# Kernel optimization log

Measured on AMD Instinct MI355X. Metric: run time of the kernel, lower is better.

Reference implementation:

```python
import jax, jax.numpy as jnp
import numpy as np

DEPTH, HEADS, DIM_HEAD, DIM, MLP, PATCH_DIM, NP_, NC = 8, 8, 64, 512, 2048, 512, 1024, 2
INNER = HEADS * DIM_HEAD
SCALE = DIM_HEAD ** -0.5
EPS = 1e-5

def layernorm(x, s, b):
    m = x.mean(-1, keepdims=True)
    v = ((x - m) ** 2).mean(-1, keepdims=True)
    return (x - m) * jax.lax.rsqrt(v + EPS) * s + b

def setup_inputs() -> dict:
    key = jax.random.key(0)
    ks = jax.random.split(key, 24)
    g = lambda k, sh, sc=0.02: jax.random.normal(k, sh, dtype=jnp.float32) * sc
    return {
        "img": jax.random.normal(ks[0], (4, NP_, PATCH_DIM), dtype=jnp.float32),
        "embed_w": g(ks[1], (PATCH_DIM, DIM)), "embed_b": jnp.zeros((DIM,), jnp.float32),
        "pos_emb": g(ks[2], (1, NP_ + 1, DIM), 1.0), "cls_token": g(ks[3], (1, 1, DIM), 1.0),
        "ln1_s": jnp.ones((DEPTH, DIM), jnp.float32), "ln1_b": jnp.zeros((DEPTH, DIM), jnp.float32),
        "qkv_w": g(ks[4], (DEPTH, DIM, 3 * INNER)),
        "out_w": g(ks[5], (DEPTH, INNER, DIM)), "out_b": jnp.zeros((DEPTH, DIM), jnp.float32),
        "ln2_s": jnp.ones((DEPTH, DIM), jnp.float32), "ln2_b": jnp.zeros((DEPTH, DIM), jnp.float32),
        "ff_w1": g(ks[6], (DEPTH, DIM, MLP)), "ff_b1": jnp.zeros((DEPTH, MLP), jnp.float32),
        "ff_w2": g(ks[7], (DEPTH, MLP, DIM)), "ff_b2": jnp.zeros((DEPTH, DIM), jnp.float32),
        "head_ln_s": jnp.ones((DIM,), jnp.float32), "head_ln_b": jnp.zeros((DIM,), jnp.float32),
        "head_w": g(ks[8], (DIM, NC)), "head_b": jnp.zeros((NC,), jnp.float32),
    }

def reference(img, embed_w, embed_b, pos_emb, cls_token, ln1_s, ln1_b, qkv_w, out_w, out_b,
              ln2_s, ln2_b, ff_w1, ff_b1, ff_w2, ff_b2, head_ln_s, head_ln_b, head_w, head_b):
    B, N, _ = img.shape
    x = img @ embed_w + embed_b                       # [B, N, DIM]
    cls = jnp.broadcast_to(cls_token, (B, 1, DIM))
    x = jnp.concatenate([cls, x], axis=1) + pos_emb[:, :N + 1]
    for l in range(DEPTH):
        h = layernorm(x, ln1_s[l], ln1_b[l])
        qkv = h @ qkv_w[l]                            # [B, N+1, 3*INNER]
        q, k, v = jnp.split(qkv, 3, axis=-1)
        rh = lambda t: t.reshape(B, N + 1, HEADS, DIM_HEAD).transpose(0, 2, 1, 3)
        q, k, v = rh(q), rh(k), rh(v)                 # [B, H, N+1, Dh]
        dots = jnp.einsum('bhnd,bhmd->bhnm', q, k) * SCALE
        attn = jax.nn.softmax(dots, axis=-1)
        o = jnp.einsum('bhnm,bhmd->bhnd', attn, v)
        o = o.transpose(0, 2, 1, 3).reshape(B, N + 1, INNER)
        x = o @ out_w[l] + out_b[l] + x
        h = layernorm(x, ln2_s[l], ln2_b[l])
        h = jax.nn.gelu(h @ ff_w1[l] + ff_b1[l], approximate=False)
        x = h @ ff_w2[l] + ff_b2[l] + x
    x = x[:, 0]                                       # cls pooling
    x = layernorm(x, head_ln_s, head_ln_b)
    return (jax.nn.sigmoid(x @ head_w + head_b),)
```

## Files before the change

kernel.cpp:

```cpp
#include <hip/hip_runtime.h>
#include <math.h>
#include <stdint.h>

#define NHEADS   8
#define DHEAD    64
#define DIMM     512
#define MLPD     2048
#define NPATCH   1024
#define NTOK     1025
#define BATCH    4
#define ROWS     (BATCH*NTOK)
#define TOKPAD   1088
#define NCHUNK   17
#define CSPLIT   9
#define QSC      0.180336881f
#define LN_EPS   1e-5f

typedef __attribute__((ext_vector_type(8))) short short8;
typedef __attribute__((ext_vector_type(4))) float f32x4;

__device__ __forceinline__ unsigned short f2bf(float f) {
  union { float f; unsigned u; } c; c.f = f;
  unsigned u = c.u;
  return (unsigned short)((u + 0x7fffu + ((u >> 16) & 1u)) >> 16);
}
__device__ __forceinline__ unsigned short f2bf_fast(float f) {
  union { float f; unsigned u; } c; c.f = f;
  return (unsigned short)((c.u + 0x8000u) >> 16);
}
__device__ __forceinline__ float bf2f(unsigned short b) {
  union { unsigned u; float f; } c; c.u = (unsigned)b << 16;
  return c.f;
}

__device__ __forceinline__ float wsum(float v) {
#pragma unroll
  for (int o = 32; o > 0; o >>= 1) v += __shfl_xor(v, o, 64);
  return v;
}

__device__ __forceinline__ void gl_lds16(const void* g, const void* l) {
  __builtin_amdgcn_global_load_lds(
      (const __attribute__((address_space(1))) unsigned int*)(uintptr_t)g,
      (__attribute__((address_space(3))) unsigned int*)(unsigned int)(uintptr_t)l,
      16, 0, 0);
}

template <int TM, int TN, int WR, int WC, bool ACOMB>
__global__ __launch_bounds__(256) void mgemm_k(
    const unsigned short* __restrict__ A, const unsigned short* __restrict__ Bt,
    const float* __restrict__ bias, const float* __restrict__ res,
    void* __restrict__ Cout, int M, int N, int K, int flags,
    unsigned short* __restrict__ vTout, const float* __restrict__ mlc,
    const float* __restrict__ posp)
{
  constexpr int AF = TM / WR / 16;
  constexpr int BF = TN / WC / 16;
  constexpr int AG = TM / 32;
  constexpr int BG = TN / 32;
  __shared__ unsigned short sA[2][TM * 64];
  __shared__ unsigned short sB[2][TN * 64];
  const int tid = threadIdx.x;
  const int w = tid >> 6, lane = tid & 63;
  const int quad = lane >> 4, l15 = lane & 15;
  const int m0 = blockIdx.y * TM, n0 = blockIdx.x * TN;
  const int wrow = (w / WC) * (TM / WR);
  const int wcol = (w % WC) * (TN / WC);
  const int lrow = lane >> 3;
  const int lkg = (lane & 7) ^ lrow;

  size_t abase[AG], bbase[BG];
  int arow[AG];
#pragma unroll
  for (int g = 0; g < AG; g++) {
    int grp = w * AG + g;
    int ar = m0 + grp * 8 + lrow; ar = ar < M ? ar : M - 1;
    arow[g] = ar;
    abase[g] = (size_t)ar * K + lkg * 8;
  }
#pragma unroll
  for (int g = 0; g < BG; g++) {
    int grp = w * BG + g;
    int br = n0 + grp * 8 + lrow;
    bbase[g] = (size_t)br * K + lkg * 8;
  }

  auto stageB = [&](int k0, int buf) {
#pragma unroll
    for (int g = 0; g < BG; g++)
      gl_lds16(Bt + bbase[g] + k0, &sB[buf][(w * BG + g) * 512]);
  };
  auto stageA_dma = [&](int k0, int buf) {
#pragma unroll
    for (int g = 0; g < AG; g++)
      gl_lds16(A + abase[g] + k0, &sA[buf][(w * AG + g) * 512]);
  };

  uint4 ra0[AG], ra1[AG];
  float rl0[AG], rl1[AG];
  auto loadAC = [&](int k0) {
    const int h = k0 >> 6;
#pragma unroll
    for (int g = 0; g < AG; g++) {
      size_t off = abase[g] + k0;
      ra0[g] = *(const uint4*)(A + off);
      ra1[g] = *(const uint4*)(A + (size_t)ROWS * DIMM + off);
      int b = arow[g] / NTOK, tok = arow[g] - b * NTOK;
      int bh = b * 8 + h;
      rl0[g] = mlc[(size_t)bh * NTOK + tok];
      rl1[g] = mlc[(size_t)(32 + bh) * NTOK + tok];
    }
  };
  auto writeAC = [&](int buf) {
#pragma unroll
    for (int g = 0; g < AG; g++) {
      float inv = 1.0f / (rl0[g] + rl1[g]);
      const unsigned short* p0 = (const unsigned short*)&ra0[g];
      const unsigned short* p1 = (const unsigned short*)&ra1[g];
      alignas(16) unsigned short o[8];
#pragma unroll
      for (int i = 0; i < 8; i++)
        o[i] = f2bf((bf2f(p0[i]) + bf2f(p1[i])) * inv);
      *(uint4*)&sA[buf][(w * AG + g) * 512 + lane * 8] = *(const uint4*)o;
    }
  };

  f32x4 acc[AF][BF];
#pragma unroll
  for (int i = 0; i < AF; i++)
#pragma unroll
    for (int j = 0; j < BF; j++) { f32x4 z = {0.f, 0.f, 0.f, 0.f}; acc[i][j] = z; }

  if (ACOMB) { stageB(0, 0); loadAC(0); writeAC(0); }
  else       { stageA_dma(0, 0); stageB(0, 0); }

  const int nsteps = K >> 6;
  for (int step = 0; step < nsteps; step++) {
    const int buf = step & 1;
    __syncthreads();
    if (step + 1 < nsteps) {
      stageB((step + 1) << 6, buf ^ 1);
      if (ACOMB) loadAC((step + 1) << 6);
      else       stageA_dma((step + 1) << 6, buf ^ 1);
    }
#pragma unroll
    for (int kk = 0; kk < 2; kk++) {
      short8 af[AF], bfr[BF];
#pragma unroll
      for (int i = 0; i < AF; i++) {
        int r = wrow + i * 16 + l15;
        af[i] = *(const short8*)&sA[buf][r * 64 + (((kk * 4 + quad) ^ (lane & 7)) << 3)];
      }
#pragma unroll
      for (int j = 0; j < BF; j++) {
        int r = wcol + j * 16 + l15;
        bfr[j] = *(const short8*)&sB[buf][r * 64 + (((kk * 4 + quad) ^ (lane & 7)) << 3)];
      }
#pragma unroll
      for (int i = 0; i < AF; i++)
#pragma unroll
        for (int j = 0; j < BF; j++)
          acc[i][j] = __builtin_amdgcn_mfma_f32_16x16x32_bf16(af[i], bfr[j], acc[i][j], 0, 0, 0);
    }
    if (ACOMB && step + 1 < nsteps) writeAC(buf ^ 1);
  }

  const bool do_gelu = flags & 1;
  const bool out_bf  = flags & 2;
  const bool embedf  = flags & 4;
#pragma unroll
  for (int i = 0; i < AF; i++) {
#pragma unroll
    for (int j = 0; j < BF; j++) {
      const int col = n0 + wcol + j * 16 + l15;
      const bool vcol = (vTout != nullptr) && (col >= 1024);
      alignas(8) unsigned short vb[4];
#pragma unroll
      for (int rg = 0; rg < 4; rg++) {
        int row = m0 + wrow + i * 16 + quad * 4 + rg;
        if (row >= M) continue;
        float v = acc[i][j][rg];
        if (bias) v += bias[col];
        if (do_gelu) v = 0.5f * v * (1.0f + erff(v * 0.70710678118654752f));
        if (res) v += res[(size_t)row * N + col];
        if (embedf) {
          int bb = row >> 10, t = (row & 1023) + 1;
          ((float*)Cout)[((size_t)(bb * NTOK + t)) * N + col] =
              v + posp[(size_t)t * N + col];
        } else if (out_bf) {
          unsigned short bv = f2bf(v);
          vb[rg] = bv;
          if (!vcol) ((unsigned short*)Cout)[(size_t)row * N + col] = bv;
        } else {
          ((float*)Cout)[(size_t)row * N + col] = v;
        }
      }
      if (vcol) {
        const int hcol = col - 1024, h = hcol >> 6, d = hcol & 63;
#pragma unroll
        for (int rg = 0; rg < 4; rg++) {
          int row = m0 + wrow + i * 16 + quad * 4 + rg;
          if (row >= M) continue;
          int bb = row / NTOK, tok = row - bb * NTOK;
          vTout[((size_t)(bb * 8 + h) * 64 + d) * TOKPAD + tok] = vb[rg];
        }
      }
    }
  }
}

__global__ __launch_bounds__(256) void attn_k(
    const unsigned short* __restrict__ qkv, const unsigned short* __restrict__ vT,
    unsigned short* __restrict__ po, float* __restrict__ ml)
{
  __shared__ unsigned short ps[64 * 64];
  __shared__ unsigned short ks[2][64 * 64];
  __shared__ unsigned short vs[2][64 * 64];
  const int bh = blockIdx.x, b = bh >> 3, h = bh & 7;
  const int q0 = blockIdx.y * 64;
  const int split = blockIdx.z;
  const int tid = threadIdx.x, w = tid >> 6, lane = tid & 63;
  const int quad = lane >> 4, l15 = lane & 15;
  const int lrow = lane >> 3, lkg = (lane & 7) ^ lrow;
  const unsigned short* qbase = qkv + (size_t)(b * NTOK) * 1536 + h * 64;
  const unsigned short* kbase = qbase + 512;
  const unsigned short* vtb   = vT + (size_t)bh * 64 * TOKPAD;

  auto stage_kv = [&](int c0, int buf) {
#pragma unroll
    for (int g = 0; g < 2; g++) {
      int grp = w * 2 + g;
      int tok = c0 + grp * 8 + lrow; tok = tok < NTOK ? tok : NTOK - 1;
      gl_lds16(kbase + (size_t)tok * 1536 + lkg * 8, &ks[buf][grp * 512]);
      int d = grp * 8 + lrow;
      gl_lds16(vtb + (size_t)d * TOKPAD + c0 + lkg * 8, &vs[buf][grp * 512]);
    }
  };

  const int cbeg = split ? CSPLIT : 0;
  const int cend = split ? NCHUNK : CSPLIT;
  stage_kv(cbeg * 64, 0);

  int qr = q0 + w * 16 + l15; qr = qr < NTOK ? qr : NTOK - 1;
  const unsigned short* qrow = qbase + (size_t)qr * 1536;
  short8 aq[2];
  aq[0] = *(const short8*)(qrow + quad * 8);
  aq[1] = *(const short8*)(qrow + 32 + quad * 8);
#pragma unroll
  for (int k = 0; k < 2; k++)
#pragma unroll
    for (int i = 0; i < 8; i++)
      aq[k][i] = (short)f2bf(bf2f((unsigned short)aq[k][i]) * QSC);

  short8 ones;
#pragma unroll
  for (int i = 0; i < 8; i++) ones[i] = (short)0x3F80;

  f32x4 Oa[4];
#pragma unroll
  for (int n = 0; n < 4; n++) { f32x4 z = {0.f, 0.f, 0.f, 0.f}; Oa[n] = z; }
  float lst[4] = {0.f, 0.f, 0.f, 0.f};

  for (int c = cbeg; c < cend; c++) {
    const int c0 = c * 64;
    const int buf = (c - cbeg) & 1;
    __syncthreads();
    if (c + 1 < cend) stage_kv(c0 + 64, buf ^ 1);

    f32x4 sa[4];
#pragma unroll
    for (int n = 0; n < 4; n++) {
      f32x4 s = {0.f, 0.f, 0.f, 0.f};
#pragma unroll
      for (int kk = 0; kk < 2; kk++) {
        short8 bk = *(const short8*)&ks[buf][(n * 16 + l15) * 64 + (((kk * 4 + quad) ^ (lane & 7)) << 3)];
        s = __builtin_amdgcn_mfma_f32_16x16x32_bf16(aq[kk], bk, s, 0, 0, 0);
      }
      sa[n] = s;
    }

    if (c0 + 64 > NTOK) {
#pragma unroll
      for (int n = 0; n < 4; n++) {
        bool oob = (c0 + n * 16 + l15) >= NTOK;
#pragma unroll
        for (int rg = 0; rg < 4; rg++)
          if (oob) sa[n][rg] = -1e30f;
      }
    }

#pragma unroll
    for (int n = 0; n < 4; n++)
#pragma unroll
      for (int rg = 0; rg < 4; rg++) {
        int row = w * 16 + quad * 4 + rg;
        int key = n * 16 + l15;
        ps[row * 64 + ((((key >> 3) ^ (row & 7)) & 7) << 3) + (key & 7)] =
            f2bf_fast(exp2f(sa[n][rg]));
      }

    short8 ap[2];
#pragma unroll
    for (int kk = 0; kk < 2; kk++)
      ap[kk] = *(const short8*)&ps[(w * 16 + l15) * 64 + (((kk * 4 + quad) ^ (lane & 7)) << 3)];

    f32x4 lsum = {0.f, 0.f, 0.f, 0.f};
#pragma unroll
    for (int kk = 0; kk < 2; kk++)
      lsum = __builtin_amdgcn_mfma_f32_16x16x32_bf16(ap[kk], ones, lsum, 0, 0, 0);
#pragma unroll
    for (int rg = 0; rg < 4; rg++) lst[rg] += lsum[rg];

#pragma unroll
    for (int n = 0; n < 4; n++) {
      f32x4 o = Oa[n];
#pragma unroll
      for (int kk = 0; kk < 2; kk++) {
        short8 bv = *(const short8*)&vs[buf][(n * 16 + l15) * 64 + (((kk * 4 + quad) ^ (lane & 7)) << 3)];
        o = __builtin_amdgcn_mfma_f32_16x16x32_bf16(ap[kk], bv, o, 0, 0, 0);
      }
      Oa[n] = o;
    }
  }

  unsigned short* pob = po + (size_t)split * ROWS * DIMM;
#pragma unroll
  for (int n = 0; n < 4; n++)
#pragma unroll
    for (int rg = 0; rg < 4; rg++) {
      int tok = q0 + w * 16 + quad * 4 + rg;
      if (tok < NTOK)
        pob[(size_t)(b * NTOK + tok) * DIMM + h * 64 + n * 16 + l15] = f2bf(Oa[n][rg]);
    }
  if (l15 == 0) {
#pragma unroll
    for (int rg = 0; rg < 4; rg++) {
      int tok = q0 + w * 16 + quad * 4 + rg;
      if (tok < NTOK)
        ml[(size_t)(split * 32 + bh) * NTOK + tok] = lst[rg];
    }
  }
}

__global__ __launch_bounds__(256) void ln_k(
    const float* __restrict__ X, const float* __restrict__ s,
    const float* __restrict__ b, unsigned short* __restrict__ Y, int nrows)
{
  const int w = threadIdx.x >> 6, lane = threadIdx.x & 63;
  const int row = blockIdx.x * 4 + w;
  if (row >= nrows) return;
  const float* x = X + (size_t)row * DIMM;
  float4 v0 = *(const float4*)(x + lane * 8);
  float4 v1 = *(const float4*)(x + lane * 8 + 4);
  float xv[8] = {v0.x, v0.y, v0.z, v0.w, v1.x, v1.y, v1.z, v1.w};
  float sum = 0.f, sq = 0.f;
#pragma unroll
  for (int i = 0; i < 8; i++) { sum += xv[i]; sq += xv[i] * xv[i]; }
  sum = wsum(sum); sq = wsum(sq);
  const float mean = sum * (1.0f / DIMM);
  const float var  = sq * (1.0f / DIMM) - mean * mean;
  const float r    = rsqrtf(var + LN_EPS);
  alignas(16) unsigned short tmp[8];
#pragma unroll
  for (int i = 0; i < 8; i++) {
    int d = lane * 8 + i;
    tmp[i] = f2bf((xv[i] - mean) * r * s[d] + b[d]);
  }
  *(uint4*)&Y[(size_t)row * DIMM + lane * 8] = *(const uint4*)tmp;
}

#define CLS_B   8
#define IMG_B   2048
#define TC0     (CLS_B + IMG_B)
#define TQKV    (TC0 + 256)
#define TOUT    (TQKV + 6144)
#define TFF1    (TOUT + 2048)
#define TFF2    (TFF1 + 8192)
#define TEND    (TFF2 + 8192)

__global__ __launch_bounds__(256) void prep_k(
    const float* __restrict__ embed_w, const float* __restrict__ qkv_w,
    const float* __restrict__ out_w, const float* __restrict__ ff1_w,
    const float* __restrict__ ff2_w,
    unsigned short* __restrict__ wt_embed, unsigned short* __restrict__ wt_qkv,
    unsigned short* __restrict__ wt_out, unsigned short* __restrict__ wt_ff1,
    unsigned short* __restrict__ wt_ff2,
    const float* __restrict__ img, unsigned short* __restrict__ img_bf,
    const float* __restrict__ cls, const float* __restrict__ pos,
    float* __restrict__ x)
{
  __shared__ float tl[32][33];
  const int bid = blockIdx.x, tid = threadIdx.x;
  if (bid < CLS_B) {
    int idx = bid * 256 + tid;
    int b = idx >> 9, d = idx & 511;
    x[(size_t)b * NTOK * DIMM + d] = cls[d] + pos[d];
    return;
  }
  if (bid < TC0) {
    int i = (bid - CLS_B) * 256 + tid;
    float4 v = ((const float4*)img)[i];
    alignas(8) unsigned short o[4] = {f2bf(v.x), f2bf(v.y), f2bf(v.z), f2bf(v.w)};
    ((uint2*)img_bf)[i] = *(const uint2*)o;
    return;
  }
  const float* W; unsigned short* Wt; int K, N, t;
  if (bid < TQKV)      { W = embed_w; Wt = wt_embed; K = 512;  N = 512;  t = bid - TC0;  }
  else if (bid < TOUT) { W = qkv_w;   Wt = wt_qkv;   K = 512;  N = 1536; t = bid - TQKV; }
  else if (bid < TFF1) { W = out_w;   Wt = wt_out;   K = 512;  N = 512;  t = bid - TOUT; }
  else if (bid < TFF2) { W = ff1_w;   Wt = wt_ff1;   K = 512;  N = 2048; t = bid - TFF1; }
  else                 { W = ff2_w;   Wt = wt_ff2;   K = 2048; N = 512;  t = bid - TFF2; }
  const int ntx = N >> 5;
  const int tpz = ntx * (K >> 5);
  const int z = t / tpz, r = t - z * tpz;
  const int n0 = (r % ntx) << 5, k0 = (r / ntx) << 5;
  const size_t off = (size_t)z * K * N;
  const float* Wz = W + off;
  unsigned short* Wtz = Wt + off;
  const int tx = tid & 31, ty = tid >> 5;
#pragma unroll
  for (int i = 0; i < 4; i++)
    tl[ty + 8 * i][tx] = Wz[(size_t)(k0 + ty + 8 * i) * N + n0 + tx];
  __syncthreads();
#pragma unroll
  for (int i = 0; i < 4; i++) {
    int n = ty + 8 * i;
    Wtz[(size_t)(n0 + n) * K + k0 + tx] = f2bf(tl[tx][n]);
  }
}

__global__ __launch_bounds__(256) void head_k(
    const float* __restrict__ X, const float* __restrict__ s,
    const float* __restrict__ bln, const float* __restrict__ W,
    const float* __restrict__ bh, float* __restrict__ out)
{
  const int w = threadIdx.x >> 6, lane = threadIdx.x & 63;
  if (w >= BATCH) return;
  const float* x = X + (size_t)w * NTOK * DIMM;
  float4 v0 = *(const float4*)(x + lane * 8);
  float4 v1 = *(const float4*)(x + lane * 8 + 4);
  float xv[8] = {v0.x, v0.y, v0.z, v0.w, v1.x, v1.y, v1.z, v1.w};
  float sum = 0.f, sq = 0.f;
#pragma unroll
  for (int i = 0; i < 8; i++) { sum += xv[i]; sq += xv[i] * xv[i]; }
  sum = wsum(sum); sq = wsum(sq);
  const float mean = sum * (1.0f / DIMM);
  const float var  = sq * (1.0f / DIMM) - mean * mean;
  const float r    = rsqrtf(var + LN_EPS);
  float l0 = 0.f, l1 = 0.f;
#pragma unroll
  for (int i = 0; i < 8; i++) {
    int d = lane * 8 + i;
    float xn = (xv[i] - mean) * r * s[d] + bln[d];
    l0 = fmaf(xn, W[d * 2 + 0], l0);
    l1 = fmaf(xn, W[d * 2 + 1], l1);
  }
  l0 = wsum(l0); l1 = wsum(l1);
  if (lane == 0) {
    out[w * 2 + 0] = 1.0f / (1.0f + expf(-(l0 + bh[0])));
    out[w * 2 + 1] = 1.0f / (1.0f + expf(-(l1 + bh[1])));
  }
}

extern "C" void kernel_launch(void* const* d_in, const int* in_sizes, int n_in,
                              void* d_out, int out_size, void* d_ws, size_t ws_size,
                              hipStream_t stream)
{
  const float* img       = (const float*)d_in[0];
  const float* embed_w   = (const float*)d_in[1];
  const float* embed_b   = (const float*)d_in[2];
  const float* pos_emb   = (const float*)d_in[3];
  const float* cls_token = (const float*)d_in[4];
  const float* ln1_s     = (const float*)d_in[5];
  const float* ln1_b     = (const float*)d_in[6];
  const float* qkv_w     = (const float*)d_in[7];
  const float* out_w     = (const float*)d_in[8];
  const float* out_b     = (const float*)d_in[9];
  const float* ln2_s     = (const float*)d_in[10];
  const float* ln2_b     = (const float*)d_in[11];
  const float* ff_w1     = (const float*)d_in[12];
  const float* ff_b1     = (const float*)d_in[13];
  const float* ff_w2     = (const float*)d_in[14];
  const float* ff_b2     = (const float*)d_in[15];
  const float* head_ln_s = (const float*)d_in[16];
  const float* head_ln_b = (const float*)d_in[17];
  const float* head_w    = (const float*)d_in[18];
  const float* head_b    = (const float*)d_in[19];
  float* out = (float*)d_out;

  char* p = (char*)d_ws;
  auto alloc = [&](size_t bytes) { char* r = p; p += (bytes + 255) & ~(size_t)255; return r; };

  unsigned short* wt_embed = (unsigned short*)alloc((size_t)512 * 512 * 2);
  unsigned short* wt_qkv   = (unsigned short*)alloc((size_t)8 * 1536 * 512 * 2);
  unsigned short* wt_out   = (unsigned short*)alloc((size_t)8 * 512 * 512 * 2);
  unsigned short* wt_ff1   = (unsigned short*)alloc((size_t)8 * 2048 * 512 * 2);
  unsigned short* wt_ff2   = (unsigned short*)alloc((size_t)8 * 512 * 2048 * 2);
  unsigned short* img_bf   = (unsigned short*)alloc((size_t)4096 * 512 * 2);
  float*          x        = (float*)alloc((size_t)ROWS * DIMM * 4);
  unsigned short* h        = (unsigned short*)alloc((size_t)ROWS * DIMM * 2);
  unsigned short* vTb      = (unsigned short*)alloc((size_t)32 * 64 * TOKPAD * 2);
  unsigned short* po       = (unsigned short*)alloc((size_t)2 * ROWS * DIMM * 2);
  float*          mlb      = (float*)alloc((size_t)2 * 32 * NTOK * 4);
  char*           big      = alloc((size_t)ROWS * MLPD * 2);
  unsigned short* qkvb     = (unsigned short*)big;
  unsigned short* ffh      = (unsigned short*)big;

  dim3 blk(256);

  prep_k<<<TEND, blk, 0, stream>>>(
      embed_w, qkv_w, out_w, ff_w1, ff_w2,
      wt_embed, wt_qkv, wt_out, wt_ff1, wt_ff2,
      img, img_bf, cls_token, pos_emb, x);

  mgemm_k<32, 64, 2, 2, false><<<dim3(8, 128), blk, 0, stream>>>(
      img_bf, wt_embed, embed_b, nullptr, x, 4096, 512, 512, 4,
      nullptr, nullptr, pos_emb);

  const int mt32 = (ROWS + 31) / 32;
  for (int l = 0; l < 8; l++) {
    ln_k<<<(ROWS + 3) / 4, blk, 0, stream>>>(
        x, ln1_s + l * DIMM, ln1_b + l * DIMM, h, ROWS);
    mgemm_k<32, 64, 2, 2, false><<<dim3(24, mt32), blk, 0, stream>>>(
        h, wt_qkv + (size_t)l * 1536 * 512, nullptr, nullptr,
        qkvb, ROWS, 1536, 512, 2, vTb, nullptr, nullptr);
    attn_k<<<dim3(32, 17, 2), blk, 0, stream>>>(qkvb, vTb, po, mlb);
    mgemm_k<32, 64, 2, 2, true><<<dim3(8, mt32), blk, 0, stream>>>(
        po, wt_out + (size_t)l * 512 * 512, out_b + l * DIMM, x,
        x, ROWS, 512, 512, 0, nullptr, mlb, nullptr);
    ln_k<<<(ROWS + 3) / 4, blk, 0, stream>>>(
        x, ln2_s + l * DIMM, ln2_b + l * DIMM, h, ROWS);
    mgemm_k<32, 64, 2, 2, false><<<dim3(32, mt32), blk, 0, stream>>>(
        h, wt_ff1 + (size_t)l * 2048 * 512, ff_b1 + l * MLPD, nullptr,
        ffh, ROWS, 2048, 512, 1 | 2, nullptr, nullptr, nullptr);
    mgemm_k<32, 64, 2, 2, false><<<dim3(8, mt32), blk, 0, stream>>>(
        ffh, wt_ff2 + (size_t)l * 512 * 2048, ff_b2 + l * DIMM, x,
        x, ROWS, 512, 2048, 0, nullptr, nullptr, nullptr);
  }

  head_k<<<1, blk, 0, stream>>>(x, head_ln_s, head_ln_b, head_w, head_b, out);
}
```

Before: 1.211 ms.

## Remap attention grid for XCD locality and vectorize weight transpose in prep

The attention launch becomes a 1D grid whose block index is decoded so that blocks sharing the same batch-head group land on the same XCD (bid&7), which should improve L2 reuse of K/V across query tiles. The weight prep kernel now handles 128x32 tiles with float4 loads and 16-byte bf16 stores instead of scalar 32x32 tiles, cutting the block count and the number of memory transactions. The wider LDS tile uses padding 129, which may still cause bank conflicts on the column writes.

```diff
diff --git a/kernel.cpp b/kernel.cpp
--- a/kernel.cpp
+++ b/kernel.cpp
@@ -216,9 +216,13 @@
   __shared__ unsigned short ps[64 * 64];
   __shared__ unsigned short ks[2][64 * 64];
   __shared__ unsigned short vs[2][64 * 64];
-  const int bh = blockIdx.x, b = bh >> 3, h = bh & 7;
-  const int q0 = blockIdx.y * 64;
-  const int split = blockIdx.z;
+  const int bid = blockIdx.x;
+  const int g8 = bid & 7, ii = bid >> 3;
+  const int bh = (g8 << 2) | (ii & 3);
+  const int rest = ii >> 2;
+  const int q0 = (rest % 17) * 64;
+  const int split = rest / 17;
+  const int b = bh >> 3, h = bh & 7;
   const int tid = threadIdx.x, w = tid >> 6, lane = tid & 63;
   const int quad = lane >> 4, l15 = lane & 15;
   const int lrow = lane >> 3, lkg = (lane & 7) ^ lrow;
@@ -372,11 +376,11 @@
 #define CLS_B   8
 #define IMG_B   2048
 #define TC0     (CLS_B + IMG_B)
-#define TQKV    (TC0 + 256)
-#define TOUT    (TQKV + 6144)
-#define TFF1    (TOUT + 2048)
-#define TFF2    (TFF1 + 8192)
-#define TEND    (TFF2 + 8192)
+#define TQKV    (TC0 + 64)
+#define TOUT    (TQKV + 1536)
+#define TFF1    (TOUT + 512)
+#define TFF2    (TFF1 + 2048)
+#define TEND    (TFF2 + 2048)
 
 __global__ __launch_bounds__(256) void prep_k(
     const float* __restrict__ embed_w, const float* __restrict__ qkv_w,
@@ -389,7 +393,7 @@
     const float* __restrict__ cls, const float* __restrict__ pos,
     float* __restrict__ x)
 {
-  __shared__ float tl[32][33];
+  __shared__ float tl[32][129];
   const int bid = blockIdx.x, tid = threadIdx.x;
   if (bid < CLS_B) {
     int idx = bid * 256 + tid;
@@ -411,21 +415,29 @@
   else if (bid < TFF2) { W = ff1_w;   Wt = wt_ff1;   K = 512;  N = 2048; t = bid - TFF1; }
   else                 { W = ff2_w;   Wt = wt_ff2;   K = 2048; N = 512;  t = bid - TFF2; }
   const int ntx = N >> 5;
-  const int tpz = ntx * (K >> 5);
+  const int tpz = ntx * (K >> 7);
   const int z = t / tpz, r = t - z * tpz;
-  const int n0 = (r % ntx) << 5, k0 = (r / ntx) << 5;
+  const int n0 = (r % ntx) << 5, k0 = (r / ntx) << 7;
   const size_t off = (size_t)z * K * N;
   const float* Wz = W + off;
   unsigned short* Wtz = Wt + off;
-  const int tx = tid & 31, ty = tid >> 5;
-#pragma unroll
-  for (int i = 0; i < 4; i++)
-    tl[ty + 8 * i][tx] = Wz[(size_t)(k0 + ty + 8 * i) * N + n0 + tx];
+#pragma unroll
+  for (int it = 0; it < 4; it++) {
+    int lin = it * 256 + tid;
+    int k = lin >> 3, f4 = (lin & 7) << 2;
+    float4 v = *(const float4*)&Wz[(size_t)(k0 + k) * N + n0 + f4];
+    tl[f4 + 0][k] = v.x; tl[f4 + 1][k] = v.y;
+    tl[f4 + 2][k] = v.z; tl[f4 + 3][k] = v.w;
+  }
   __syncthreads();
-#pragma unroll
-  for (int i = 0; i < 4; i++) {
-    int n = ty + 8 * i;
-    Wtz[(size_t)(n0 + n) * K + k0 + tx] = f2bf(tl[tx][n]);
+  const int n = tid >> 3, kg = tid & 7;
+#pragma unroll
+  for (int j = 0; j < 2; j++) {
+    int kb = kg * 16 + j * 8;
+    alignas(16) unsigned short o[8];
+#pragma unroll
+    for (int i = 0; i < 8; i++) o[i] = f2bf(tl[n][kb + i]);
+    *(uint4*)&Wtz[(size_t)(n0 + n) * K + k0 + kb] = *(const uint4*)o;
   }
 }
 
@@ -524,7 +536,7 @@
     mgemm_k<32, 64, 2, 2, false><<<dim3(24, mt32), blk, 0, stream>>>(
         h, wt_qkv + (size_t)l * 1536 * 512, nullptr, nullptr,
         qkvb, ROWS, 1536, 512, 2, vTb, nullptr, nullptr);
-    attn_k<<<dim3(32, 17, 2), blk, 0, stream>>>(qkvb, vTb, po, mlb);
+    attn_k<<<dim3(1088), blk, 0, stream>>>(qkvb, vTb, po, mlb);
     mgemm_k<32, 64, 2, 2, true><<<dim3(8, mt32), blk, 0, stream>>>(
         po, wt_out + (size_t)l * 512 * 512, out_b + l * DIMM, x,
         x, ROWS, 512, 512, 0, nullptr, mlb, nullptr);
```

Measured after the change: 1.190 ms. No clear change (-1.8%).
